# Performance work log

Hardware: AMD Instinct MI355X
Metric: run time of the kernel (lower is better)

The kernel has to match this reference:

```python
import jax, jax.numpy as jnp
import numpy as np

S, B, T, D = 256, 32, 24, 512


def setup_inputs() -> dict:
    key = jax.random.key(0)
    ks = jax.random.split(key, 30)
    def lin(k, out_d, in_d):
        kw, kb = jax.random.split(k)
        w = jax.random.normal(kw, (out_d, in_d), jnp.float32) * 0.02
        b = jax.random.normal(kb, (out_d,), jnp.float32) * 0.02
        return w, b
    inp = {
        'context_output': jax.random.normal(ks[0], (S, B, D), jnp.float32),
        'context_hidden_state': jax.random.normal(ks[1], (B, D), jnp.float32),
        'question_output': jax.random.normal(ks[2], (T, B, D), jnp.float32),
        'question_hidden_state': jax.random.normal(ks[3], (B, D), jnp.float32),
        'image_output': jax.random.normal(ks[4], (S, B, D), jnp.float32),
        'image_hidden_state': jax.random.normal(ks[5], (B, D), jnp.float32),
    }
    inp['fc1_w'], inp['fc1_b'] = lin(ks[6], D, D)
    inp['fc2_w'], inp['fc2_b'] = lin(ks[7], D, D)
    inp['dm_w'], inp['dm_b'] = lin(ks[8], D, D)
    inp['ms_w'], inp['ms_b'] = lin(ks[9], 1, D)
    inp['rm_w'], inp['rm_b'] = lin(ks[10], D, D)
    inp['qm_w'], inp['qm_b'] = lin(ks[11], D, D)
    inp['rr_w'], inp['rr_b'] = lin(ks[12], D, D)
    inp['rg_w'], inp['rg_b'] = lin(ks[13], D, D)
    inp['qg_w'], inp['qg_b'] = lin(ks[14], D, D)
    return inp


def reference(context_output, context_hidden_state, question_output,
              question_hidden_state, image_output, image_hidden_state,
              fc1_w, fc1_b, fc2_w, fc2_b, dm_w, dm_b, ms_w, ms_b,
              rm_w, rm_b, qm_w, qm_b, rr_w, rr_b, rg_w, rg_b, qg_w, qg_b):
    # context_output/image_output: [S,B,D] -> co: [B,S,D]
    co = (jnp.einsum('sbd,ed->bse', context_output, fc1_w) + fc1_b
          + jnp.einsum('sbd,ed->bse', image_output, fc2_w) + fc2_b)
    # linear_dm(co) is loop-invariant; compute once (same math as original)
    co_dm = jnp.einsum('bsd,ed->bse', co, dm_w) + dm_b  # [B,S,D]

    def step(r, q):
        # r: [B,D] (the original's [B,1,D] memory), q: [B,D]
        add = (r @ rm_w.T + rm_b) + (q @ qm_w.T + qm_b)  # [B,D]
        m = jnp.tanh(co_dm + add[:, None, :])             # [B,S,D]
        logits = m @ ms_w.T + ms_b                        # [B,S,1]
        s = jax.nn.softmax(logits, axis=1)                # softmax over S
        r_new = jnp.sum(s * co, axis=1) + jnp.tanh(r @ rr_w.T + rr_b)
        return r_new, None

    r0 = jnp.zeros((B, D), co.dtype)
    r, _ = jax.lax.scan(step, r0, question_output)  # scan over T steps
    g = (r @ rg_w.T + rg_b) + (question_hidden_state @ qg_w.T + qg_b)
    return g
```

## Files before the change

kernel.cpp:

```cpp
#include <hip/hip_runtime.h>

#define S_DIM 256
#define B_DIM 32
#define T_DIM 24
#define D_DIM 512

typedef short short8 __attribute__((ext_vector_type(8)));
typedef unsigned short ushort8 __attribute__((ext_vector_type(8)));
typedef unsigned short ushort4v __attribute__((ext_vector_type(4)));
typedef float float4v __attribute__((ext_vector_type(4)));

#define ATOM_ST(p, v) __hip_atomic_store((p), (v), __ATOMIC_RELAXED, __HIP_MEMORY_SCOPE_AGENT)
#define ATOM_LD(p)    __hip_atomic_load((p), __ATOMIC_RELAXED, __HIP_MEMORY_SCOPE_AGENT)

__device__ __forceinline__ float bf2f(unsigned short u) {
  union { unsigned int i; float f; } v; v.i = ((unsigned int)u) << 16; return v.f;
}
__device__ __forceinline__ unsigned short f2bf(float f) {
  union { float f; unsigned int i; } v; v.f = f;
  unsigned int i = v.i;
  return (unsigned short)((i + 0x7fffu + ((i >> 16) & 1u)) >> 16);
}
__device__ __forceinline__ float tanh_fast(float x) {
  float p = __builtin_amdgcn_exp2f(x * 2.885390082f);
  return 1.f - 2.f * __builtin_amdgcn_rcpf(1.f + p);
}

__device__ __forceinline__ void gload_lds16(const void* g, void* l) {
  __builtin_amdgcn_global_load_lds(
      (const __attribute__((address_space(1))) void*)g,
      (__attribute__((address_space(3))) void*)l, 16, 0, 0);
}

__global__ __launch_bounds__(256)
void cvt_kernel(const float* __restrict__ s0, const float* __restrict__ s1,
                const float* __restrict__ s2, const float* __restrict__ s3,
                const float* __restrict__ s4, const float* __restrict__ s5,
                const float* __restrict__ s6,
                unsigned short* __restrict__ d0, unsigned short* __restrict__ d1,
                unsigned short* __restrict__ d2, unsigned short* __restrict__ d3,
                unsigned short* __restrict__ d4, unsigned short* __restrict__ d5,
                unsigned short* __restrict__ d6)
{
  const int idx = blockIdx.x * 256 + threadIdx.x;
  const float* s; unsigned short* d; int off;
  if (idx < 2097152) {
    off = idx & 1048575;
    if (idx < 1048576) { s = s0; d = d0; } else { s = s1; d = d1; }
  } else if (idx < 2195456) {
    off = idx - 2097152; s = s2; d = d2;
  } else {
    const int k = (idx - 2195456) >> 16;
    off = (idx - 2195456) & 65535;
    switch (k) {
      case 0:  s = s3; d = d3; break;
      case 1:  s = s4; d = d4; break;
      case 2:  s = s5; d = d5; break;
      default: s = s6; d = d6; break;
    }
  }
  const float4v v = ((const float4v*)s)[off];
  ushort4v u;
  u[0] = f2bf(v[0]); u[1] = f2bf(v[1]); u[2] = f2bf(v[2]); u[3] = f2bf(v[3]);
  ((ushort4v*)d)[off] = u;
}

template<bool DUAL, bool OUT_BF16, bool PERMUTE>
__global__ __launch_bounds__(256)
void gemm_nt(const unsigned short* __restrict__ A1,
             const unsigned short* __restrict__ A2,
             const unsigned short* __restrict__ W1,
             const unsigned short* __restrict__ W2,
             const float* __restrict__ bias1,
             const float* __restrict__ bias2,
             void* __restrict__ out)
{
  __shared__ unsigned short At[128 * 32] __attribute__((aligned(16)));
  __shared__ unsigned short Bt[128 * 32] __attribute__((aligned(16)));

  const int tid  = threadIdx.x;
  const int wid  = tid >> 6;
  const int lane = tid & 63;
  const int bm = blockIdx.x, bn = blockIdx.y;
  const int wm = (wid & 1) * 64, wn = (wid >> 1) * 64;

  float4v acc[4][4];
#pragma unroll
  for (int i = 0; i < 4; ++i)
#pragma unroll
    for (int jj = 0; jj < 4; ++jj) acc[i][jj] = (float4v){0.f, 0.f, 0.f, 0.f};

  const int NK = DUAL ? 32 : 16;
  for (int it = 0; it < NK; ++it) {
    const int kk = it * 32;
    const unsigned short* As = A1;
    const unsigned short* Ws = W1;
    int ks = kk;
    if (DUAL && kk >= 512) { As = A2; Ws = W2; ks = kk - 512; }

    __syncthreads();
#pragma unroll
    for (int i = 0; i < 2; ++i) {
      const int lrow = wid * 32 + i * 16 + (lane >> 2);
      const int kc = (lane & 3) * 8;
      gload_lds16(As + (size_t)(bm * 128 + lrow) * 512 + ks + kc,
                  &At[(wid * 32 + i * 16) * 32]);
      gload_lds16(Ws + (size_t)(bn * 128 + lrow) * 512 + ks + kc,
                  &Bt[(wid * 32 + i * 16) * 32]);
    }
    __syncthreads();

    short8 fa[4], fb[4];
#pragma unroll
    for (int mi = 0; mi < 4; ++mi)
      fa[mi] = *(const short8*)&At[(wm + mi * 16 + (lane & 15)) * 32 + (lane >> 4) * 8];
#pragma unroll
    for (int ni = 0; ni < 4; ++ni)
      fb[ni] = *(const short8*)&Bt[(wn + ni * 16 + (lane & 15)) * 32 + (lane >> 4) * 8];
#pragma unroll
    for (int mi = 0; mi < 4; ++mi)
#pragma unroll
      for (int ni = 0; ni < 4; ++ni)
        acc[mi][ni] = __builtin_amdgcn_mfma_f32_16x16x32_bf16(fa[mi], fb[ni], acc[mi][ni], 0, 0, 0);
  }

#pragma unroll
  for (int mi = 0; mi < 4; ++mi) {
    const int row0 = wm + mi * 16 + (lane >> 4) * 4;
#pragma unroll
    for (int ni = 0; ni < 4; ++ni) {
      const int col = bn * 128 + wn + ni * 16 + (lane & 15);
      float bsum = 0.f;
      if (bias1) bsum += bias1[col];
      if (bias2) bsum += bias2[col];
#pragma unroll
      for (int i = 0; i < 4; ++i) {
        const int m = bm * 128 + row0 + i;
        const int orow = PERMUTE ? ((m & 31) * 256 + (m >> 5)) : m;
        const float v = acc[mi][ni][i] + bsum;
        if (OUT_BF16) ((unsigned short*)out)[(size_t)orow * 512 + col] = f2bf(v);
        else          ((float*)out)[(size_t)orow * 512 + col] = v;
      }
    }
  }
}

__global__ __launch_bounds__(512)
void scan_kernel(const unsigned short* __restrict__ co,
                 const unsigned short* __restrict__ codm,
                 const float* __restrict__ qadd,
                 float* __restrict__ addB,
                 float* __restrict__ rrtB,
                 float* __restrict__ denB,
                 float* __restrict__ pvecB,
                 unsigned int* __restrict__ cnt,
                 const float* __restrict__ ms_w,
                 const float* __restrict__ rm_w,
                 const float* __restrict__ rr_w,
                 const float* __restrict__ rr_b,
                 const float* __restrict__ qhs,
                 const float* __restrict__ rg_w,
                 const float* __restrict__ qg_w,
                 const float* __restrict__ rg_b,
                 const float* __restrict__ qg_b,
                 float* __restrict__ outg)
{
  __shared__ unsigned short scrS[32 * 520] __attribute__((aligned(16)));
  __shared__ float rS[512];
  __shared__ float addS[512] __attribute__((aligned(16)));
  __shared__ float msS[512] __attribute__((aligned(16)));
  __shared__ float partS[512];
  __shared__ float partR[512];
  __shared__ float wS[32];
  __shared__ float rrbS[64];

  const int tid  = threadIdx.x;
  const int wid  = tid >> 6;
  const int lane = tid & 63;
  const int b = blockIdx.x >> 3;
  const int j = blockIdx.x & 7;
  unsigned int* cntb = cnt + b * 16;

  ushort8 rmp[8], rrp[8];
  for (int pass = 0; pass < 4; ++pass) {
    const float* Wsrc = (pass < 2) ? rm_w : rr_w;
    const int rbase = (pass & 1) * 32;
    for (int r = wid; r < 32; r += 8) {
      const float* src = &Wsrc[(size_t)(j * 64 + rbase + r) * 512 + lane * 8];
      float4v a = *(const float4v*)src;
      float4v c = *(const float4v*)(src + 4);
      ushort8 u8;
#pragma unroll
      for (int i = 0; i < 4; ++i) { u8[i] = f2bf(a[i]); u8[i + 4] = f2bf(c[i]); }
      *(ushort8*)&scrS[r * 520 + lane * 8] = u8;
    }
    __syncthreads();
    if ((lane >> 5) == (pass & 1)) {
      const int rloc = lane & 31;
#pragma unroll
      for (int u = 0; u < 8; ++u) {
        ushort8 v = *(const ushort8*)&scrS[rloc * 520 + wid * 64 + u * 8];
        if (pass < 2) rmp[u] = v; else rrp[u] = v;
      }
    }
    __syncthreads();
  }

  const size_t gbase = ((size_t)b * 256 + j * 32) * 512;
  for (int idx = tid; idx < 2048; idx += 512)
    *(ushort8*)&scrS[idx * 8] = *(const ushort8*)&codm[gbase + (size_t)idx * 8];
  const unsigned short* cdS = scrS;

  msS[tid] = ms_w[tid];
  if (tid < 64) rrbS[tid] = rr_b[j * 64 + tid];
  rS[tid] = 0.f;
  __syncthreads();

  for (int t = 0; t < T_DIM; ++t) {
    float am = 0.f, ar = 0.f;
#pragma unroll
    for (int u = 0; u < 8; ++u) {
      ushort8 wm8 = rmp[u], wr8 = rrp[u];
#pragma unroll
      for (int i2 = 0; i2 < 8; ++i2) {
        const float rv = rS[wid * 64 + u * 8 + i2];
        am = fmaf(rv, bf2f(wm8[i2]), am);
        ar = fmaf(rv, bf2f(wr8[i2]), ar);
      }
    }
    partS[wid * 64 + lane] = am;
    partR[wid * 64 + lane] = ar;
    __syncthreads();
    if (wid == 0) {
      float s = 0.f;
#pragma unroll
      for (int w2 = 0; w2 < 8; ++w2) s += partS[w2 * 64 + lane];
      s += qadd[((size_t)t * 32 + b) * 512 + j * 64 + lane];
      ATOM_ST(&addB[b * 512 + j * 64 + lane], s);
    } else if (wid == 1) {
      float s = 0.f;
#pragma unroll
      for (int w2 = 0; w2 < 8; ++w2) s += partR[w2 * 64 + lane];
      ATOM_ST(&rrtB[(t & 1) * (B_DIM * 512) + b * 512 + j * 64 + lane],
              tanh_fast(s + rrbS[lane]));
    }
    __syncthreads();
    if (tid == 0) {
      __hip_atomic_fetch_add(cntb, 1u, __ATOMIC_RELAXED, __HIP_MEMORY_SCOPE_AGENT);
      const unsigned int tgt = 8u * (2u * (unsigned)t + 1u);
      while (ATOM_LD(cntb) < tgt) __builtin_amdgcn_s_sleep(2);
    }
    __syncthreads();

    addS[tid] = ATOM_LD(&addB[b * 512 + tid]);
    __syncthreads();
#pragma unroll
    for (int q = 0; q < 4; ++q) {
      const int sl = wid * 4 + q;
      ushort8 cd8 = *(const ushort8*)&cdS[sl * 512 + lane * 8];
      float4v a0 = *(const float4v*)&addS[lane * 8];
      float4v a1 = *(const float4v*)&addS[lane * 8 + 4];
      float4v m0 = *(const float4v*)&msS[lane * 8];
      float4v m1 = *(const float4v*)&msS[lane * 8 + 4];
      float acc = 0.f;
#pragma unroll
      for (int i = 0; i < 4; ++i) {
        acc = fmaf(tanh_fast(bf2f(cd8[i]) + a0[i]), m0[i], acc);
        acc = fmaf(tanh_fast(bf2f(cd8[i + 4]) + a1[i]), m1[i], acc);
      }
#pragma unroll
      for (int off = 32; off > 0; off >>= 1) acc += __shfl_xor(acc, off, 64);
      if (lane == 0) wS[sl] = __builtin_amdgcn_exp2f(acc * 1.44269504f);
    }
    __syncthreads();

    {
      float accv = 0.f;
#pragma unroll 8
      for (int sl = 0; sl < 32; ++sl)
        accv = fmaf(wS[sl], bf2f(co[gbase + (size_t)sl * 512 + tid]), accv);
      ATOM_ST(&pvecB[((size_t)b * 8 + j) * 512 + tid], accv);
      if (tid == 0) {
        float dsum = 0.f;
        for (int sl = 0; sl < 32; ++sl) dsum += wS[sl];
        ATOM_ST(&denB[b * 8 + j], dsum);
      }
    }
    __syncthreads();
    if (tid == 0) {
      __hip_atomic_fetch_add(cntb, 1u, __ATOMIC_RELAXED, __HIP_MEMORY_SCOPE_AGENT);
      const unsigned int tgt = 8u * (2u * (unsigned)t + 2u);
      while (ATOM_LD(cntb) < tgt) __builtin_amdgcn_s_sleep(2);
    }
    __syncthreads();

    {
      float sum = 0.f;
#pragma unroll
      for (int jj = 0; jj < 8; ++jj)
        sum += ATOM_LD(&pvecB[((size_t)b * 8 + jj) * 512 + tid]);
      float den = 0.f;
#pragma unroll
      for (int jj = 0; jj < 8; ++jj) den += ATOM_LD(&denB[b * 8 + jj]);
      rS[tid] = sum * __builtin_amdgcn_rcpf(den) +
                ATOM_LD(&rrtB[(t & 1) * (B_DIM * 512) + b * 512 + tid]);
    }
    __syncthreads();
  }

  addS[tid] = qhs[b * 512 + tid];
  __syncthreads();
  {
    const int e = j * 64 + lane;
    const float* rgp = rg_w + (size_t)e * 512 + wid * 64;
    const float* qgp = qg_w + (size_t)e * 512 + wid * 64;
    float acc = 0.f;
#pragma unroll
    for (int u = 0; u < 8; ++u) {
      float4v g0 = *(const float4v*)&rgp[u * 8];
      float4v g1 = *(const float4v*)&rgp[u * 8 + 4];
      float4v q0 = *(const float4v*)&qgp[u * 8];
      float4v q1 = *(const float4v*)&qgp[u * 8 + 4];
#pragma unroll
      for (int i2 = 0; i2 < 4; ++i2) {
        acc = fmaf(rS[wid * 64 + u * 8 + i2],     g0[i2], acc);
        acc = fmaf(rS[wid * 64 + u * 8 + 4 + i2], g1[i2], acc);
        acc = fmaf(addS[wid * 64 + u * 8 + i2],     q0[i2], acc);
        acc = fmaf(addS[wid * 64 + u * 8 + 4 + i2], q1[i2], acc);
      }
    }
    partS[wid * 64 + lane] = acc;
  }
  __syncthreads();
  if (wid == 0) {
    float s = 0.f;
#pragma unroll
    for (int w2 = 0; w2 < 8; ++w2) s += partS[w2 * 64 + lane];
    const int e = j * 64 + lane;
    s += rg_b[e] + qg_b[e];
    outg[b * 512 + e] = s;
  }
}

extern "C" void kernel_launch(void* const* d_in, const int* in_sizes, int n_in,
                              void* d_out, int out_size, void* d_ws, size_t ws_size,
                              hipStream_t stream)
{
  (void)in_sizes; (void)n_in; (void)out_size; (void)ws_size;
  const float* ctx  = (const float*)d_in[0];
  const float* qo   = (const float*)d_in[2];
  const float* qhs  = (const float*)d_in[3];
  const float* img  = (const float*)d_in[4];
  const float* fc1w = (const float*)d_in[6];
  const float* fc1b = (const float*)d_in[7];
  const float* fc2w = (const float*)d_in[8];
  const float* fc2b = (const float*)d_in[9];
  const float* dmw  = (const float*)d_in[10];
  const float* dmb  = (const float*)d_in[11];
  const float* msw  = (const float*)d_in[12];
  const float* rmw  = (const float*)d_in[14];
  const float* rmb  = (const float*)d_in[15];
  const float* qmw  = (const float*)d_in[16];
  const float* qmb  = (const float*)d_in[17];
  const float* rrw  = (const float*)d_in[18];
  const float* rrb  = (const float*)d_in[19];
  const float* rgw  = (const float*)d_in[20];
  const float* rgb  = (const float*)d_in[21];
  const float* qgw  = (const float*)d_in[22];
  const float* qgb  = (const float*)d_in[23];

  char* ws = (char*)d_ws;
  unsigned int* cnt    = (unsigned int*)ws;
  unsigned short* co   = (unsigned short*)(ws + 4096);
  unsigned short* codm = co + (size_t)B_DIM * S_DIM * D_DIM;
  float* qadd = (float*)(codm + (size_t)B_DIM * S_DIM * D_DIM);
  float* addB = qadd + (size_t)T_DIM * B_DIM * D_DIM;
  float* rrtB = addB + B_DIM * D_DIM;
  float* denB = rrtB + 2 * B_DIM * D_DIM;
  float* pvecB = denB + 256;
  unsigned short* ctxb  = (unsigned short*)(pvecB + B_DIM * 8 * D_DIM);
  unsigned short* imgb  = ctxb + (size_t)S_DIM * B_DIM * D_DIM;
  unsigned short* qob   = imgb + (size_t)S_DIM * B_DIM * D_DIM;
  unsigned short* fc1wb = qob + (size_t)T_DIM * B_DIM * D_DIM;
  unsigned short* fc2wb = fc1wb + D_DIM * D_DIM;
  unsigned short* dmwb  = fc2wb + D_DIM * D_DIM;
  unsigned short* qmwb  = dmwb + D_DIM * D_DIM;

  hipMemsetAsync(cnt, 0, 4096, stream);
  cvt_kernel<<<9600, 256, 0, stream>>>(ctx, img, qo, fc1w, fc2w, dmw, qmw,
                                       ctxb, imgb, qob, fc1wb, fc2wb, dmwb, qmwb);
  gemm_nt<true, true, true><<<dim3(64, 4), 256, 0, stream>>>(ctxb, imgb, fc1wb, fc2wb, fc1b, fc2b, (void*)co);
  gemm_nt<false, true, false><<<dim3(64, 4), 256, 0, stream>>>(co, nullptr, dmwb, nullptr, dmb, nullptr, (void*)codm);
  gemm_nt<false, false, false><<<dim3(6, 4), 256, 0, stream>>>(qob, nullptr, qmwb, nullptr, qmb, rmb, (void*)qadd);
  scan_kernel<<<256, 512, 0, stream>>>(co, codm, qadd, addB, rrtB, denB, pvecB, cnt,
                                       msw, rmw, rrw, rrb, qhs, rgw, qgw, rgb, qgb,
                                       (float*)d_out);
}
```

Measured before the change: 386.6 us.

## Fuse bf16 conversion into GEMM loads, move qm projection into scan, use tagged flags

Drops the separate fp32-to-bf16 conversion kernel: the GEMMs now read fp32 inputs and weights directly and convert while staging into LDS. The question projection GEMM is folded into the scan kernel's prologue, using per-block qm weights held in registers. The counter-based inter-block barriers are replaced by 64-bit tag+value flags that consumers poll individually, removing the atomic counter round trips and two syncthreads per phase. The cost is fp32 global loads through registers instead of direct LDS loads, a larger scan prologue, and a bigger memset for the tag buffers.

```diff
diff --git a/kernel.cpp b/kernel.cpp
--- a/kernel.cpp
+++ b/kernel.cpp
@@ -7,11 +7,11 @@
 
 typedef short short8 __attribute__((ext_vector_type(8)));
 typedef unsigned short ushort8 __attribute__((ext_vector_type(8)));
-typedef unsigned short ushort4v __attribute__((ext_vector_type(4)));
 typedef float float4v __attribute__((ext_vector_type(4)));
-
-#define ATOM_ST(p, v) __hip_atomic_store((p), (v), __ATOMIC_RELAXED, __HIP_MEMORY_SCOPE_AGENT)
-#define ATOM_LD(p)    __hip_atomic_load((p), __ATOMIC_RELAXED, __HIP_MEMORY_SCOPE_AGENT)
+typedef unsigned long long u64;
+
+#define ATOM_ST64(p, v) __hip_atomic_store((p), (v), __ATOMIC_RELAXED, __HIP_MEMORY_SCOPE_AGENT)
+#define ATOM_LD64(p)    __hip_atomic_load((p), __ATOMIC_RELAXED, __HIP_MEMORY_SCOPE_AGENT)
 
 __device__ __forceinline__ float bf2f(unsigned short u) {
   union { unsigned int i; float f; } v; v.i = ((unsigned int)u) << 16; return v.f;
@@ -25,55 +25,31 @@
   float p = __builtin_amdgcn_exp2f(x * 2.885390082f);
   return 1.f - 2.f * __builtin_amdgcn_rcpf(1.f + p);
 }
-
 __device__ __forceinline__ void gload_lds16(const void* g, void* l) {
   __builtin_amdgcn_global_load_lds(
       (const __attribute__((address_space(1))) void*)g,
       (__attribute__((address_space(3))) void*)l, 16, 0, 0);
 }
-
+__device__ __forceinline__ u64 pack_tag(unsigned tag, float v) {
+  union { float f; unsigned u; } c; c.f = v;
+  return ((u64)tag << 32) | (u64)c.u;
+}
+__device__ __forceinline__ float unpack_val(u64 v) {
+  union { unsigned u; float f; } c; c.u = (unsigned)v; return c.f;
+}
+__device__ __forceinline__ float poll_val(const u64* p, unsigned tag) {
+  u64 v = ATOM_LD64(p);
+  while ((unsigned)(v >> 32) != tag) { __builtin_amdgcn_s_sleep(1); v = ATOM_LD64(p); }
+  return unpack_val(v);
+}
+
+template<bool A_F32, bool W_F32, bool DUAL, bool PERMUTE>
 __global__ __launch_bounds__(256)
-void cvt_kernel(const float* __restrict__ s0, const float* __restrict__ s1,
-                const float* __restrict__ s2, const float* __restrict__ s3,
-                const float* __restrict__ s4, const float* __restrict__ s5,
-                const float* __restrict__ s6,
-                unsigned short* __restrict__ d0, unsigned short* __restrict__ d1,
-                unsigned short* __restrict__ d2, unsigned short* __restrict__ d3,
-                unsigned short* __restrict__ d4, unsigned short* __restrict__ d5,
-                unsigned short* __restrict__ d6)
-{
-  const int idx = blockIdx.x * 256 + threadIdx.x;
-  const float* s; unsigned short* d; int off;
-  if (idx < 2097152) {
-    off = idx & 1048575;
-    if (idx < 1048576) { s = s0; d = d0; } else { s = s1; d = d1; }
-  } else if (idx < 2195456) {
-    off = idx - 2097152; s = s2; d = d2;
-  } else {
-    const int k = (idx - 2195456) >> 16;
-    off = (idx - 2195456) & 65535;
-    switch (k) {
-      case 0:  s = s3; d = d3; break;
-      case 1:  s = s4; d = d4; break;
-      case 2:  s = s5; d = d5; break;
-      default: s = s6; d = d6; break;
-    }
-  }
-  const float4v v = ((const float4v*)s)[off];
-  ushort4v u;
-  u[0] = f2bf(v[0]); u[1] = f2bf(v[1]); u[2] = f2bf(v[2]); u[3] = f2bf(v[3]);
-  ((ushort4v*)d)[off] = u;
-}
-
-template<bool DUAL, bool OUT_BF16, bool PERMUTE>
-__global__ __launch_bounds__(256)
-void gemm_nt(const unsigned short* __restrict__ A1,
-             const unsigned short* __restrict__ A2,
-             const unsigned short* __restrict__ W1,
-             const unsigned short* __restrict__ W2,
+void gemm_nt(const void* __restrict__ A1v, const void* __restrict__ A2v,
+             const void* __restrict__ W1v, const void* __restrict__ W2v,
              const float* __restrict__ bias1,
              const float* __restrict__ bias2,
-             void* __restrict__ out)
+             unsigned short* __restrict__ out)
 {
   __shared__ unsigned short At[128 * 32] __attribute__((aligned(16)));
   __shared__ unsigned short Bt[128 * 32] __attribute__((aligned(16)));
@@ -93,20 +69,51 @@
   const int NK = DUAL ? 32 : 16;
   for (int it = 0; it < NK; ++it) {
     const int kk = it * 32;
-    const unsigned short* As = A1;
-    const unsigned short* Ws = W1;
+    const void* Av = A1v;
+    const void* Wv = W1v;
     int ks = kk;
-    if (DUAL && kk >= 512) { As = A2; Ws = W2; ks = kk - 512; }
-
-    __syncthreads();
-#pragma unroll
-    for (int i = 0; i < 2; ++i) {
-      const int lrow = wid * 32 + i * 16 + (lane >> 2);
-      const int kc = (lane & 3) * 8;
-      gload_lds16(As + (size_t)(bm * 128 + lrow) * 512 + ks + kc,
-                  &At[(wid * 32 + i * 16) * 32]);
-      gload_lds16(Ws + (size_t)(bn * 128 + lrow) * 512 + ks + kc,
-                  &Bt[(wid * 32 + i * 16) * 32]);
+    if (DUAL && kk >= 512) { Av = A2v; Wv = W2v; ks = kk - 512; }
+
+    __syncthreads();
+    if (A_F32) {
+      const float* Af = (const float*)Av;
+      const int r = tid >> 1, h = tid & 1;
+      const float4v* p = (const float4v*)(Af + (size_t)(bm * 128 + r) * 512 + ks + h * 16);
+      float4v x0 = p[0], x1 = p[1], x2 = p[2], x3 = p[3];
+      ushort8 u0, u1;
+#pragma unroll
+      for (int i = 0; i < 4; ++i) {
+        u0[i] = f2bf(x0[i]); u0[i + 4] = f2bf(x1[i]);
+        u1[i] = f2bf(x2[i]); u1[i + 4] = f2bf(x3[i]);
+      }
+      *(ushort8*)&At[r * 32 + h * 16] = u0;
+      *(ushort8*)&At[r * 32 + h * 16 + 8] = u1;
+    } else {
+      const unsigned short* Ab = (const unsigned short*)Av;
+#pragma unroll
+      for (int i = 0; i < 2; ++i)
+        gload_lds16(Ab + (size_t)(bm * 128 + wid * 32 + i * 16 + (lane >> 2)) * 512 + ks + (lane & 3) * 8,
+                    &At[(wid * 32 + i * 16) * 32]);
+    }
+    if (W_F32) {
+      const float* Wf = (const float*)Wv;
+      const int r = tid >> 1, h = tid & 1;
+      const float4v* p = (const float4v*)(Wf + (size_t)(bn * 128 + r) * 512 + ks + h * 16);
+      float4v x0 = p[0], x1 = p[1], x2 = p[2], x3 = p[3];
+      ushort8 u0, u1;
+#pragma unroll
+      for (int i = 0; i < 4; ++i) {
+        u0[i] = f2bf(x0[i]); u0[i + 4] = f2bf(x1[i]);
+        u1[i] = f2bf(x2[i]); u1[i + 4] = f2bf(x3[i]);
+      }
+      *(ushort8*)&Bt[r * 32 + h * 16] = u0;
+      *(ushort8*)&Bt[r * 32 + h * 16 + 8] = u1;
+    } else {
+      const unsigned short* Wb = (const unsigned short*)Wv;
+#pragma unroll
+      for (int i = 0; i < 2; ++i)
+        gload_lds16(Wb + (size_t)(bn * 128 + wid * 32 + i * 16 + (lane >> 2)) * 512 + ks + (lane & 3) * 8,
+                    &Bt[(wid * 32 + i * 16) * 32]);
     }
     __syncthreads();
 
@@ -137,9 +144,7 @@
       for (int i = 0; i < 4; ++i) {
         const int m = bm * 128 + row0 + i;
         const int orow = PERMUTE ? ((m & 31) * 256 + (m >> 5)) : m;
-        const float v = acc[mi][ni][i] + bsum;
-        if (OUT_BF16) ((unsigned short*)out)[(size_t)orow * 512 + col] = f2bf(v);
-        else          ((float*)out)[(size_t)orow * 512 + col] = v;
+        out[(size_t)orow * 512 + col] = f2bf(acc[mi][ni][i] + bsum);
       }
     }
   }
@@ -148,16 +153,18 @@
 __global__ __launch_bounds__(512)
 void scan_kernel(const unsigned short* __restrict__ co,
                  const unsigned short* __restrict__ codm,
-                 const float* __restrict__ qadd,
-                 float* __restrict__ addB,
-                 float* __restrict__ rrtB,
-                 float* __restrict__ denB,
-                 float* __restrict__ pvecB,
-                 unsigned int* __restrict__ cnt,
+                 const float* __restrict__ qo,
+                 u64* __restrict__ addT,
+                 u64* __restrict__ rrtT,
+                 u64* __restrict__ denT,
+                 u64* __restrict__ pvecT,
                  const float* __restrict__ ms_w,
                  const float* __restrict__ rm_w,
                  const float* __restrict__ rr_w,
                  const float* __restrict__ rr_b,
+                 const float* __restrict__ qm_w,
+                 const float* __restrict__ qm_b,
+                 const float* __restrict__ rm_b,
                  const float* __restrict__ qhs,
                  const float* __restrict__ rg_w,
                  const float* __restrict__ qg_w,
@@ -173,17 +180,19 @@
   __shared__ float partR[512];
   __shared__ float wS[32];
   __shared__ float rrbS[64];
+  __shared__ float qmrmS[64];
+  __shared__ float denS[8];
+  __shared__ float qaddS[T_DIM * 64];
 
   const int tid  = threadIdx.x;
   const int wid  = tid >> 6;
   const int lane = tid & 63;
   const int b = blockIdx.x >> 3;
   const int j = blockIdx.x & 7;
-  unsigned int* cntb = cnt + b * 16;
-
-  ushort8 rmp[8], rrp[8];
-  for (int pass = 0; pass < 4; ++pass) {
-    const float* Wsrc = (pass < 2) ? rm_w : rr_w;
+
+  ushort8 rmp[8], rrp[8], qmp[8];
+  for (int pass = 0; pass < 6; ++pass) {
+    const float* Wsrc = (pass < 2) ? rm_w : (pass < 4) ? rr_w : qm_w;
     const int rbase = (pass & 1) * 32;
     for (int r = wid; r < 32; r += 8) {
       const float* src = &Wsrc[(size_t)(j * 64 + rbase + r) * 512 + lane * 8];
@@ -200,23 +209,61 @@
 #pragma unroll
       for (int u = 0; u < 8; ++u) {
         ushort8 v = *(const ushort8*)&scrS[rloc * 520 + wid * 64 + u * 8];
-        if (pass < 2) rmp[u] = v; else rrp[u] = v;
-      }
-    }
-    __syncthreads();
+        if (pass < 2) rmp[u] = v; else if (pass < 4) rrp[u] = v; else qmp[u] = v;
+      }
+    }
+    __syncthreads();
+  }
+
+  msS[tid] = ms_w[tid];
+  if (tid < 64) {
+    rrbS[tid]  = rr_b[j * 64 + tid];
+    qmrmS[tid] = qm_b[j * 64 + tid] + rm_b[j * 64 + tid];
+  }
+  rS[tid] = 0.f;
+
+  float* qoS = (float*)scrS;
+  for (int half = 0; half < 2; ++half) {
+    __syncthreads();
+#pragma unroll
+    for (int i = 0; i < 3; ++i) {
+      const int f4 = tid + i * 512;
+      const int tl = f4 >> 7, c4 = f4 & 127;
+      ((float4v*)qoS)[f4] =
+          *(const float4v*)&qo[((size_t)(half * 12 + tl) * 32 + b) * 512 + c4 * 4];
+    }
+    __syncthreads();
+    for (int tl = 0; tl < 12; ++tl) {
+      float p = 0.f;
+#pragma unroll
+      for (int u = 0; u < 8; ++u) {
+        ushort8 w8 = qmp[u];
+#pragma unroll
+        for (int i2 = 0; i2 < 8; ++i2)
+          p = fmaf(qoS[tl * 512 + wid * 64 + u * 8 + i2], bf2f(w8[i2]), p);
+      }
+      partS[wid * 64 + lane] = p;
+      __syncthreads();
+      if (wid == 0) {
+        float s = 0.f;
+#pragma unroll
+        for (int w2 = 0; w2 < 8; ++w2) s += partS[w2 * 64 + lane];
+        qaddS[(half * 12 + tl) * 64 + lane] = s + qmrmS[lane];
+      }
+      __syncthreads();
+    }
   }
 
   const size_t gbase = ((size_t)b * 256 + j * 32) * 512;
   for (int idx = tid; idx < 2048; idx += 512)
     *(ushort8*)&scrS[idx * 8] = *(const ushort8*)&codm[gbase + (size_t)idx * 8];
   const unsigned short* cdS = scrS;
-
-  msS[tid] = ms_w[tid];
-  if (tid < 64) rrbS[tid] = rr_b[j * 64 + tid];
-  rS[tid] = 0.f;
   __syncthreads();
 
   for (int t = 0; t < T_DIM; ++t) {
+    const unsigned tagA = 2u * (unsigned)t + 1u;
+    const unsigned tagB = 2u * (unsigned)t + 2u;
+
     float am = 0.f, ar = 0.f;
 #pragma unroll
     for (int u = 0; u < 8; ++u) {
@@ -235,25 +282,18 @@
       float s = 0.f;
 #pragma unroll
       for (int w2 = 0; w2 < 8; ++w2) s += partS[w2 * 64 + lane];
-      s += qadd[((size_t)t * 32 + b) * 512 + j * 64 + lane];
-      ATOM_ST(&addB[b * 512 + j * 64 + lane], s);
+      s += qaddS[t * 64 + lane];
+      ATOM_ST64(&addT[b * 512 + j * 64 + lane], pack_tag(tagA, s));
     } else if (wid == 1) {
       float s = 0.f;
 #pragma unroll
       for (int w2 = 0; w2 < 8; ++w2) s += partR[w2 * 64 + lane];
-      ATOM_ST(&rrtB[(t & 1) * (B_DIM * 512) + b * 512 + j * 64 + lane],
-              tanh_fast(s + rrbS[lane]));
-    }
-    __syncthreads();
-    if (tid == 0) {
-      __hip_atomic_fetch_add(cntb, 1u, __ATOMIC_RELAXED, __HIP_MEMORY_SCOPE_AGENT);
-      const unsigned int tgt = 8u * (2u * (unsigned)t + 1u);
-      while (ATOM_LD(cntb) < tgt) __builtin_amdgcn_s_sleep(2);
-    }
-    __syncthreads();
-
-    addS[tid] = ATOM_LD(&addB[b * 512 + tid]);
-    __syncthreads();
+      ATOM_ST64(&rrtT[(size_t)(t & 1) * (B_DIM * 512) + b * 512 + j * 64 + lane],
+                pack_tag(tagA, tanh_fast(s + rrbS[lane])));
+    }
+    addS[tid] = poll_val(&addT[b * 512 + tid], tagA);
+    __syncthreads();
+
 #pragma unroll
     for (int q = 0; q < 4; ++q) {
       const int sl = wid * 4 + q;
@@ -279,32 +319,37 @@
 #pragma unroll 8
       for (int sl = 0; sl < 32; ++sl)
         accv = fmaf(wS[sl], bf2f(co[gbase + (size_t)sl * 512 + tid]), accv);
-      ATOM_ST(&pvecB[((size_t)b * 8 + j) * 512 + tid], accv);
+      ATOM_ST64(&pvecT[((size_t)b * 8 + j) * 512 + tid], pack_tag(tagB, accv));
       if (tid == 0) {
         float dsum = 0.f;
         for (int sl = 0; sl < 32; ++sl) dsum += wS[sl];
-        ATOM_ST(&denB[b * 8 + j], dsum);
-      }
-    }
-    __syncthreads();
-    if (tid == 0) {
-      __hip_atomic_fetch_add(cntb, 1u, __ATOMIC_RELAXED, __HIP_MEMORY_SCOPE_AGENT);
-      const unsigned int tgt = 8u * (2u * (unsigned)t + 2u);
-      while (ATOM_LD(cntb) < tgt) __builtin_amdgcn_s_sleep(2);
-    }
-    __syncthreads();
-
-    {
-      float sum = 0.f;
-#pragma unroll
-      for (int jj = 0; jj < 8; ++jj)
-        sum += ATOM_LD(&pvecB[((size_t)b * 8 + jj) * 512 + tid]);
-      float den = 0.f;
-#pragma unroll
-      for (int jj = 0; jj < 8; ++jj) den += ATOM_LD(&denB[b * 8 + jj]);
-      rS[tid] = sum * __builtin_amdgcn_rcpf(den) +
-                ATOM_LD(&rrtB[(t & 1) * (B_DIM * 512) + b * 512 + tid]);
-    }
+        ATOM_ST64(&denT[b * 8 + j], pack_tag(tagB, dsum));
+      }
+    }
+
+    u64 pv[8];
+#pragma unroll
+    for (int jj = 0; jj < 8; ++jj)
+      pv[jj] = ATOM_LD64(&pvecT[((size_t)b * 8 + jj) * 512 + tid]);
+    u64 rv64 = ATOM_LD64(&rrtT[(size_t)(t & 1) * (B_DIM * 512) + b * 512 + tid]);
+    if (tid < 8) denS[tid] = poll_val(&denT[b * 8 + tid], tagB);
+    float sum = 0.f;
+#pragma unroll
+    for (int jj = 0; jj < 8; ++jj) {
+      while ((unsigned)(pv[jj] >> 32) != tagB) {
+        __builtin_amdgcn_s_sleep(1);
+        pv[jj] = ATOM_LD64(&pvecT[((size_t)b * 8 + jj) * 512 + tid]);
+      }
+      sum += unpack_val(pv[jj]);
+    }
+    while ((unsigned)(rv64 >> 32) != tagA) {
+      __builtin_amdgcn_s_sleep(1);
+      rv64 = ATOM_LD64(&rrtT[(size_t)(t & 1) * (B_DIM * 512) + b * 512 + tid]);
+    }
+    __syncthreads();
+    const float den = denS[0] + denS[1] + denS[2] + denS[3] +
+                      denS[4] + denS[5] + denS[6] + denS[7];
+    rS[tid] = sum * __builtin_amdgcn_rcpf(den) + unpack_val(rv64);
     __syncthreads();
   }
 
@@ -370,29 +415,20 @@
   const float* qgb  = (const float*)d_in[23];
 
   char* ws = (char*)d_ws;
-  unsigned int* cnt    = (unsigned int*)ws;
-  unsigned short* co   = (unsigned short*)(ws + 4096);
+  u64* addT  = (u64*)ws;
+  u64* rrtT  = addT + B_DIM * 512;
+  u64* denT  = rrtT + 2 * B_DIM * 512;
+  u64* pvecT = denT + B_DIM * 8;
+  unsigned short* co   = (unsigned short*)(pvecT + (size_t)B_DIM * 8 * 512);
   unsigned short* codm = co + (size_t)B_DIM * S_DIM * D_DIM;
-  float* qadd = (float*)(codm + (size_t)B_DIM * S_DIM * D_DIM);
-  float* addB = qadd + (size_t)T_DIM * B_DIM * D_DIM;
-  float* rrtB = addB + B_DIM * D_DIM;
-  float* denB = rrtB + 2 * B_DIM * D_DIM;
-  float* pvecB = denB + 256;
-  unsigned short* ctxb  = (unsigned short*)(pvecB + B_DIM * 8 * D_DIM);
-  unsigned short* imgb  = ctxb + (size_t)S_DIM * B_DIM * D_DIM;
-  unsigned short* qob   = imgb + (size_t)S_DIM * B_DIM * D_DIM;
-  unsigned short* fc1wb = qob + (size_t)T_DIM * B_DIM * D_DIM;
-  unsigned short* fc2wb = fc1wb + D_DIM * D_DIM;
-  unsigned short* dmwb  = fc2wb + D_DIM * D_DIM;
-  unsigned short* qmwb  = dmwb + D_DIM * D_DIM;
-
-  hipMemsetAsync(cnt, 0, 4096, stream);
-  cvt_kernel<<<9600, 256, 0, stream>>>(ctx, img, qo, fc1w, fc2w, dmw, qmw,
-                                       ctxb, imgb, qob, fc1wb, fc2wb, dmwb, qmwb);
-  gemm_nt<true, true, true><<<dim3(64, 4), 256, 0, stream>>>(ctxb, imgb, fc1wb, fc2wb, fc1b, fc2b, (void*)co);
-  gemm_nt<false, true, false><<<dim3(64, 4), 256, 0, stream>>>(co, nullptr, dmwb, nullptr, dmb, nullptr, (void*)codm);
-  gemm_nt<false, false, false><<<dim3(6, 4), 256, 0, stream>>>(qob, nullptr, qmwb, nullptr, qmb, rmb, (void*)qadd);
-  scan_kernel<<<256, 512, 0, stream>>>(co, codm, qadd, addB, rrtB, denB, pvecB, cnt,
-                                       msw, rmw, rrw, rrb, qhs, rgw, qgw, rgb, qgb,
-                                       (float*)d_out);
-}
+  const size_t tagBytes = (size_t)(131072 + 262144 + 2048 + 1048576);
+
+  hipMemsetAsync(ws, 0, tagBytes, stream);
+  gemm_nt<true, true, true, true><<<dim3(64, 4), 256, 0, stream>>>(
+      ctx, img, fc1w, fc2w, fc1b, fc2b, co);
+  gemm_nt<false, true, false, false><<<dim3(64, 4), 256, 0, stream>>>(
+      co, nullptr, dmw, nullptr, dmb, nullptr, codm);
+  scan_kernel<<<256, 512, 0, stream>>>(co, codm, qo, addT, rrtT, denT, pvecT,
+                                       msw, rmw, rrw, rrb, qmw, qmb, rmb, qhs,
+                                       rgw, qgw, rgb, qgb, (float*)d_out);
+}
```

New measurement: 420.6 us. +8.8%, slower.
